# Optimization experiments

Hardware: AMD Instinct MI355X
Metric: run time of the kernel (lower is better)

Reference implementation:

```python
import jax, jax.numpy as jnp
import numpy as np

HEAD_DIM = 64
N_HEADS = 32
N_KV = 8
ROPE_BASE = 500000.0
FREQ_CONFIG = {"factor": 32.0, "low_freq_factor": 1.0, "high_freq_factor": 4.0, "original_context_length": 8192}


def _rope_tables(head_dim, theta, n_pos, fc):
    # faithful to precompute_rope_params with llama3 freq scaling
    inv_freq = 1.0 / theta ** (np.arange(0, head_dim, 2, dtype=np.float32) / head_dim)
    low_wl = fc["original_context_length"] / fc["low_freq_factor"]
    high_wl = fc["original_context_length"] / fc["high_freq_factor"]
    wavelen = 2.0 * np.pi / inv_freq
    inv_l = np.where(wavelen > low_wl, inv_freq / fc["factor"], inv_freq)
    smooth = (fc["original_context_length"] / wavelen - fc["low_freq_factor"]) / (fc["high_freq_factor"] - fc["low_freq_factor"])
    smoothed = (1.0 - smooth) * (inv_freq / fc["factor"]) + smooth * inv_freq
    med = (wavelen <= low_wl) & (wavelen >= high_wl)
    inv_freq = np.where(med, smoothed, inv_l)
    pos = np.arange(n_pos, dtype=np.float32)
    angles = pos[:, None] * inv_freq[None, :]          # [T, head_dim/2]
    angles = np.concatenate([angles, angles], axis=1)  # [T, head_dim]
    return jnp.asarray(np.cos(angles), jnp.float32), jnp.asarray(np.sin(angles), jnp.float32)


def _apply_rope(x, cos, sin):
    # x: [b, h, t, d]; cos/sin: [t, d]
    d = x.shape[-1]
    x1, x2 = x[..., : d // 2], x[..., d // 2:]
    rotated = jnp.concatenate([-x2, x1], axis=-1)
    return x * cos[None, None] + rotated * sin[None, None]


def setup_inputs() -> dict:
    key = jax.random.key(0)
    ks = jax.random.split(key, 5)
    b, t, d = 1, 2048, 2048
    s = 0.02
    return {
        "x": jax.random.normal(ks[0], (b, t, d), jnp.float32),
        "Wq": jax.random.normal(ks[1], (d, d), jnp.float32) * s,
        "Wk": jax.random.normal(ks[2], (N_KV * HEAD_DIM, d), jnp.float32) * s,
        "Wv": jax.random.normal(ks[3], (N_KV * HEAD_DIM, d), jnp.float32) * s,
        "Wo": jax.random.normal(ks[4], (d, d), jnp.float32) * s,
        "start_pos": 0,
    }


def reference(x, Wq, Wk, Wv, Wo, start_pos):
    b, t, _ = x.shape
    cos, sin = _rope_tables(HEAD_DIM, ROPE_BASE, start_pos + t, FREQ_CONFIG)
    cos, sin = cos[start_pos:start_pos + t], sin[start_pos:start_pos + t]

    q = (x @ Wq.T).reshape(b, t, N_HEADS, HEAD_DIM).transpose(0, 2, 1, 3)  # [b,H,t,d]
    k = (x @ Wk.T).reshape(b, t, N_KV, HEAD_DIM).transpose(0, 2, 1, 3)     # [b,G,t,d]
    v = (x @ Wv.T).reshape(b, t, N_KV, HEAD_DIM).transpose(0, 2, 1, 3)

    q = _apply_rope(q, cos, sin)
    k = _apply_rope(k, cos, sin)

    n_rep = N_HEADS // N_KV
    k = jnp.repeat(k, n_rep, axis=1)  # [b,H,t,d]
    v = jnp.repeat(v, n_rep, axis=1)

    scores = jnp.einsum("bhqd,bhkd->bhqk", q, k)
    causal = jnp.triu(jnp.ones((t, t), bool), k=1)
    scores = jnp.where(causal[None, None], -jnp.inf, scores) / jnp.sqrt(jnp.float32(HEAD_DIM))
    weights = jax.nn.softmax(scores, axis=-1)
    ctx = jnp.einsum("bhqk,bhkd->bhqd", weights, v)
    ctx = ctx.transpose(0, 2, 1, 3).reshape(b, t, N_HEADS * HEAD_DIM)
    return ctx @ Wo.T
```

## Files before the change

### kernel.cpp

```cpp
#include <hip/hip_runtime.h>
#include <math.h>

#define T_SEQ 2048
#define D_MODEL 2048
#define HEAD_DIM 64
#define N_HEADS 32
#define N_KV 8

using short8 = __attribute__((ext_vector_type(8))) short;
using f32x4  = __attribute__((ext_vector_type(4))) float;

#define MFMA16(a, b, c) __builtin_amdgcn_mfma_f32_16x16x32_bf16(a, b, c, 0, 0, 0)

__device__ __forceinline__ unsigned short f2bf(float f) {
    unsigned int u = __builtin_bit_cast(unsigned int, f);
    u += 0x7fff + ((u >> 16) & 1);
    return (unsigned short)(u >> 16);
}
__device__ __forceinline__ void gld_lds16(const ushort* g, ushort* l) {
    __builtin_amdgcn_global_load_lds((const __attribute__((address_space(1))) void*)g,
                                     (__attribute__((address_space(3))) void*)l, 16, 0, 0);
}

__global__ void rope_tables_kernel(float* __restrict__ cosT, float* __restrict__ sinT,
                                   const int* __restrict__ start_pos, int T) {
    int t = blockIdx.x;
    int i = threadIdx.x;
    float pos = (float)(start_pos[0] + t);
    float expo = (float)i / 32.0f;
    float inv_freq = 1.0f / powf(500000.0f, expo);
    const float two_pi = 6.283185307179586f;
    float wavelen = two_pi / inv_freq;
    const float low_wl = 8192.0f;
    const float high_wl = 2048.0f;
    float inv;
    if (wavelen > low_wl) {
        inv = inv_freq / 32.0f;
    } else if (wavelen < high_wl) {
        inv = inv_freq;
    } else {
        float smooth = (8192.0f / wavelen - 1.0f) / 3.0f;
        inv = (1.0f - smooth) * (inv_freq / 32.0f) + smooth * inv_freq;
    }
    float ang = pos * inv;
    cosT[i * T + t] = cosf(ang);
    sinT[i * T + t] = sinf(ang);
}

__global__ __launch_bounds__(256) void cast_all_kernel(
    const float* __restrict__ x, const float* __restrict__ wq,
    const float* __restrict__ wk, const float* __restrict__ wv,
    const float* __restrict__ wo,
    ushort* __restrict__ xb, ushort* __restrict__ wqb,
    ushort* __restrict__ wkb, ushort* __restrict__ wvb, ushort* __restrict__ wob) {
    int i = blockIdx.x * 256 + threadIdx.x;
    const float* src; ushort* dst; int off;
    if (i < 1048576)      { src = x;  dst = xb;  off = i; }
    else if (i < 2097152) { src = wq; dst = wqb; off = i - 1048576; }
    else if (i < 2359296) { src = wk; dst = wkb; off = i - 2097152; }
    else if (i < 2621440) { src = wv; dst = wvb; off = i - 2359296; }
    else                  { src = wo; dst = wob; off = i - 2621440; }
    float4 v = ((const float4*)src)[off];
    ushort4 o;
    o.x = f2bf(v.x); o.y = f2bf(v.y); o.z = f2bf(v.z); o.w = f2bf(v.w);
    ((ushort4*)dst)[off] = o;
}

__global__ __launch_bounds__(256) void gemm_qkv(
    const ushort* __restrict__ X, const ushort* __restrict__ Wqb,
    const ushort* __restrict__ Wkb, const ushort* __restrict__ Wvb,
    ushort* __restrict__ Qo, ushort* __restrict__ Ko, ushort* __restrict__ Vto,
    const float* __restrict__ cosT, const float* __restrict__ sinT,
    int T, int D) {
    __shared__ __align__(16) ushort As[2][2][2048];
    __shared__ __align__(16) ushort Bs[2][2][4096];
    const int tid = threadIdx.x;
    const int w = tid >> 6, l = tid & 63;
    const int m0 = blockIdx.x * 64;
    const int n0g = blockIdx.y * 128;

    const ushort* B;
    ushort* Cout;
    int n0, doRope;
    if (n0g < 2048)      { B = Wqb + (size_t)n0g * D;          Cout = Qo;  n0 = n0g;        doRope = 1; }
    else if (n0g < 2560) { B = Wkb + (size_t)(n0g - 2048) * D; Cout = Ko;  n0 = n0g - 2048; doRope = 1; }
    else                 { B = Wvb + (size_t)(n0g - 2560) * D; Cout = Vto; n0 = n0g - 2560; doRope = 0; }

    const int wm = (w >> 1) * 32, wn = (w & 1) * 64;
    const int lr = l & 15;
    const int quad = l >> 4;

    f32x4 zero = {0.f, 0.f, 0.f, 0.f};
    f32x4 acc[2][4];
#pragma unroll
    for (int i = 0; i < 2; ++i)
#pragma unroll
        for (int j = 0; j < 4; ++j) acc[i][j] = zero;

    const int srow = l >> 2;
    const int scg  = ((l & 3) ^ (srow & 3)) * 8;
    const ushort* Ag  = X + (size_t)(m0 + 16 * w + srow) * D + scg;
    const ushort* Bg0 = B + (size_t)(16 * (2 * w) + srow) * D + scg;
    const ushort* Bg1 = B + (size_t)(16 * (2 * w + 1) + srow) * D + scg;

#define GSTAGE(k0v, nb) { \
    gld_lds16(Ag  + (k0v),      &As[nb][0][w * 512]); \
    gld_lds16(Ag  + (k0v) + 32, &As[nb][1][w * 512]); \
    gld_lds16(Bg0 + (k0v),      &Bs[nb][0][(2 * w) * 512]); \
    gld_lds16(Bg0 + (k0v) + 32, &Bs[nb][1][(2 * w) * 512]); \
    gld_lds16(Bg1 + (k0v),      &Bs[nb][0][(2 * w + 1) * 512]); \
    gld_lds16(Bg1 + (k0v) + 32, &Bs[nb][1][(2 * w + 1) * 512]); }

    GSTAGE(0, 0);

    const int rsw = (quad ^ (lr & 3)) * 8;
    for (int k0 = 0; k0 < D; k0 += 64) {
        const int b = (k0 >> 6) & 1;
        __syncthreads();
        if (k0 + 64 < D) GSTAGE(k0 + 64, b ^ 1);
#pragma unroll
        for (int sub = 0; sub < 2; ++sub) {
            short8 af[2], bf[4];
#pragma unroll
            for (int i = 0; i < 2; ++i) af[i] = *(const short8*)&As[b][sub][(wm + i * 16 + lr) * 32 + rsw];
#pragma unroll
            for (int j = 0; j < 4; ++j) bf[j] = *(const short8*)&Bs[b][sub][(wn + j * 16 + lr) * 32 + rsw];
#pragma unroll
            for (int i = 0; i < 2; ++i)
#pragma unroll
                for (int j = 0; j < 4; ++j)
                    acc[i][j] = MFMA16(af[i], bf[j], acc[i][j]);
        }
    }
#undef GSTAGE

    const int mbase = m0 + wm + quad * 4;
    if (doRope) {
#pragma unroll
        for (int i = 0; i < 2; ++i) {
            int trow = mbase + i * 16;
#pragma unroll
            for (int j = 0; j < 2; ++j) {
                int i1 = lr + j * 16;
                float4 c4 = *(const float4*)&cosT[(size_t)i1 * T + trow];
                float4 s4 = *(const float4*)&sinT[(size_t)i1 * T + trow];
                int n1 = n0 + wn + lr + j * 16;
                int n2 = n1 + 32;
                size_t b1 = (size_t)(n1 >> 6) * ((size_t)T * 64) + (size_t)(n1 & 63);
                size_t b2 = (size_t)(n2 >> 6) * ((size_t)T * 64) + (size_t)(n2 & 63);
                float cs[4] = {c4.x, c4.y, c4.z, c4.w};
                float sn[4] = {s4.x, s4.y, s4.z, s4.w};
#pragma unroll
                for (int r = 0; r < 4; ++r) {
                    float x1 = acc[i][j][r], x2 = acc[i][j + 2][r];
                    Cout[b1 + (size_t)(trow + r) * 64] = f2bf(x1 * cs[r] - x2 * sn[r]);
                    Cout[b2 + (size_t)(trow + r) * 64] = f2bf(x2 * cs[r] + x1 * sn[r]);
                }
            }
        }
    } else {
#pragma unroll
        for (int i = 0; i < 2; ++i)
#pragma unroll
            for (int j = 0; j < 4; ++j) {
                int n = n0 + wn + lr + j * 16;
                int m = mbase + i * 16;
                ushort4 o;
                o.x = f2bf(acc[i][j][0]); o.y = f2bf(acc[i][j][1]);
                o.z = f2bf(acc[i][j][2]); o.w = f2bf(acc[i][j][3]);
                *(ushort4*)&Vto[(size_t)n * T + m] = o;
            }
    }
}

__global__ __launch_bounds__(256) void gemm_bt_f32(const ushort* __restrict__ A,
                                                   const ushort* __restrict__ B,
                                                   float* __restrict__ C,
                                                   int M, int N, int K) {
    __shared__ __align__(16) ushort As[2][2][2048];
    __shared__ __align__(16) ushort Bs[2][2][4096];
    const int tid = threadIdx.x;
    const int w = tid >> 6, l = tid & 63;
    const int m0 = blockIdx.x * 64, n0 = blockIdx.y * 128;
    const int wm = (w >> 1) * 32, wn = (w & 1) * 64;
    const int lr = l & 15;
    const int quad = l >> 4;

    f32x4 zero = {0.f, 0.f, 0.f, 0.f};
    f32x4 acc[2][4];
#pragma unroll
    for (int i = 0; i < 2; ++i)
#pragma unroll
        for (int j = 0; j < 4; ++j) acc[i][j] = zero;

    const int srow = l >> 2;
    const int scg  = ((l & 3) ^ (srow & 3)) * 8;
    const ushort* Ag  = A + (size_t)(m0 + 16 * w + srow) * K + scg;
    const ushort* Bg0 = B + (size_t)(n0 + 16 * (2 * w) + srow) * K + scg;
    const ushort* Bg1 = B + (size_t)(n0 + 16 * (2 * w + 1) + srow) * K + scg;

#define GSTAGE(k0v, nb) { \
    gld_lds16(Ag  + (k0v),      &As[nb][0][w * 512]); \
    gld_lds16(Ag  + (k0v) + 32, &As[nb][1][w * 512]); \
    gld_lds16(Bg0 + (k0v),      &Bs[nb][0][(2 * w) * 512]); \
    gld_lds16(Bg0 + (k0v) + 32, &Bs[nb][1][(2 * w) * 512]); \
    gld_lds16(Bg1 + (k0v),      &Bs[nb][0][(2 * w + 1) * 512]); \
    gld_lds16(Bg1 + (k0v) + 32, &Bs[nb][1][(2 * w + 1) * 512]); }

    GSTAGE(0, 0);

    const int rsw = (quad ^ (lr & 3)) * 8;
    for (int k0 = 0; k0 < K; k0 += 64) {
        const int b = (k0 >> 6) & 1;
        __syncthreads();
        if (k0 + 64 < K) GSTAGE(k0 + 64, b ^ 1);
#pragma unroll
        for (int sub = 0; sub < 2; ++sub) {
            short8 af[2], bf[4];
#pragma unroll
            for (int i = 0; i < 2; ++i) af[i] = *(const short8*)&As[b][sub][(wm + i * 16 + lr) * 32 + rsw];
#pragma unroll
            for (int j = 0; j < 4; ++j) bf[j] = *(const short8*)&Bs[b][sub][(wn + j * 16 + lr) * 32 + rsw];
#pragma unroll
            for (int i = 0; i < 2; ++i)
#pragma unroll
                for (int j = 0; j < 4; ++j)
                    acc[i][j] = MFMA16(af[i], bf[j], acc[i][j]);
        }
    }
#undef GSTAGE

    const int mbase = m0 + wm + quad * 4;
    const int nbase = n0 + wn + lr;
#pragma unroll
    for (int i = 0; i < 2; ++i)
#pragma unroll
        for (int j = 0; j < 4; ++j)
#pragma unroll
            for (int r = 0; r < 4; ++r)
                C[(size_t)(mbase + i * 16 + r) * N + (nbase + j * 16)] = acc[i][j][r];
}

__global__ __launch_bounds__(256) void attn_mfma(const ushort* __restrict__ Q,
                                                 const ushort* __restrict__ K,
                                                 const ushort* __restrict__ Vt,
                                                 ushort* __restrict__ ctx, int T) {
    __shared__ __align__(16) ushort Ks[2][4096];
    __shared__ __align__(16) ushort Vs[2][4096];
    __shared__ __align__(16) ushort Ps[4][1152];
    const int tid = threadIdx.x, w = tid >> 6, l = tid & 63;
    const int lr = l & 15, quad = l >> 4;
    const int h = blockIdx.y, hk = h >> 2;
    const ushort* Kb = K + (size_t)hk * T * 64;
    const ushort* Vb = Vt + (size_t)hk * 64 * T;

    const int srow = l >> 3;
    const int sc   = ((l & 7) ^ srow) * 8;
    const int si0 = 2 * w, si1 = 2 * w + 1;
    const int swz = lr & 7;
    f32x4 zero = {0.f, 0.f, 0.f, 0.f};

    for (int phase = 0; phase < 2; ++phase) {
        const int qt = phase == 0 ? (31 - (int)blockIdx.x) : (int)blockIdx.x;
        const int qbase = qt * 64;
        const int qrow_abs = qbase + w * 16 + lr;
        const int ntiles = qt + 1;

        short8 qf[2];
#pragma unroll
        for (int ks = 0; ks < 2; ++ks)
            qf[ks] = *(const short8*)(Q + ((size_t)h * T + qbase + w * 16 + lr) * 64 + ks * 32 + quad * 8);

        f32x4 oacc[4];
#pragma unroll
        for (int dj = 0; dj < 4; ++dj) oacc[dj] = zero;
        float lsum = 0.f;

        gld_lds16(Kb + (size_t)(8 * si0 + srow) * 64 + sc, &Ks[0][si0 * 512]);
        gld_lds16(Kb + (size_t)(8 * si1 + srow) * 64 + sc, &Ks[0][si1 * 512]);
        gld_lds16(Vb + (size_t)(8 * si0 + srow) * T + sc, &Vs[0][si0 * 512]);
        gld_lds16(Vb + (size_t)(8 * si1 + srow) * T + sc, &Vs[0][si1 * 512]);

        for (int kt = 0; kt < ntiles; ++kt) {
            const int b = kt & 1;
            __syncthreads();
            if (kt + 1 < ntiles) {
                const int k0n = (kt + 1) * 64;
                gld_lds16(Kb + (size_t)(k0n + 8 * si0 + srow) * 64 + sc, &Ks[b ^ 1][si0 * 512]);
                gld_lds16(Kb + (size_t)(k0n + 8 * si1 + srow) * 64 + sc, &Ks[b ^ 1][si1 * 512]);
                gld_lds16(Vb + (size_t)(8 * si0 + srow) * T + k0n + sc, &Vs[b ^ 1][si0 * 512]);
                gld_lds16(Vb + (size_t)(8 * si1 + srow) * T + k0n + sc, &Vs[b ^ 1][si1 * 512]);
            }
            const int k0 = kt * 64;

            f32x4 s[4];
#pragma unroll
            for (int mi = 0; mi < 4; ++mi) s[mi] = zero;
#pragma unroll
            for (int ks = 0; ks < 2; ++ks)
#pragma unroll
                for (int mi = 0; mi < 4; ++mi) {
                    short8 kf = *(const short8*)&Ks[b][(mi * 16 + lr) * 64 + ((4 * ks + quad) ^ swz) * 8];
                    s[mi] = MFMA16(kf, qf[ks], s[mi]);
                }

            const bool masked = (kt == qt);
#pragma unroll
            for (int mi = 0; mi < 4; ++mi) {
                float pv[4];
#pragma unroll
                for (int r = 0; r < 4; ++r) {
                    float p = __expf(s[mi][r] * 0.125f);
                    if (masked && (k0 + mi * 16 + quad * 4 + r > qrow_abs)) p = 0.f;
                    lsum += p;
                    pv[r] = p;
                }
                ushort4 pk;
                pk.x = f2bf(pv[0]); pk.y = f2bf(pv[1]); pk.z = f2bf(pv[2]); pk.w = f2bf(pv[3]);
                *(ushort4*)&Ps[w][lr * 72 + mi * 16 + quad * 4] = pk;
            }

#pragma unroll
            for (int ks2 = 0; ks2 < 2; ++ks2) {
                short8 pf = *(const short8*)&Ps[w][lr * 72 + ks2 * 32 + quad * 8];
#pragma unroll
                for (int dj = 0; dj < 4; ++dj) {
                    short8 vf = *(const short8*)&Vs[b][(dj * 16 + lr) * 64 + ((4 * ks2 + quad) ^ swz) * 8];
                    oacc[dj] = MFMA16(pf, vf, oacc[dj]);
                }
            }
        }

        float v = lsum;
        v += __shfl_xor(v, 16, 64);
        v += __shfl_xor(v, 32, 64);
        float invr[4];
#pragma unroll
        for (int r = 0; r < 4; ++r)
            invr[r] = 1.f / __shfl(v, quad * 4 + r, 64);

#pragma unroll
        for (int dj = 0; dj < 4; ++dj) {
            int col = h * 64 + dj * 16 + lr;
#pragma unroll
            for (int r = 0; r < 4; ++r) {
                int row = qbase + w * 16 + quad * 4 + r;
                ctx[(size_t)row * 2048 + col] = f2bf(oacc[dj][r] * invr[r]);
            }
        }
        __syncthreads();
    }
}

extern "C" void kernel_launch(void* const* d_in, const int* in_sizes, int n_in,
                              void* d_out, int out_size, void* d_ws, size_t ws_size,
                              hipStream_t stream) {
    const float* x  = (const float*)d_in[0];
    const float* Wq = (const float*)d_in[1];
    const float* Wk = (const float*)d_in[2];
    const float* Wv = (const float*)d_in[3];
    const float* Wo = (const float*)d_in[4];
    const int* start_pos = (const int*)d_in[5];
    float* out = (float*)d_out;

    const int T = T_SEQ, D = D_MODEL;
    const int KV = N_KV * HEAD_DIM;

    char* w = (char*)d_ws;
    float* cosT = (float*)w;            w += (size_t)32 * T * 4;
    float* sinT = (float*)w;            w += (size_t)32 * T * 4;
    ushort* xbf  = (ushort*)w;          w += (size_t)T * D * 2;
    ushort* wqbf = (ushort*)w;          w += (size_t)D * D * 2;
    ushort* wkbf = (ushort*)w;          w += (size_t)KV * D * 2;
    ushort* wvbf = (ushort*)w;          w += (size_t)KV * D * 2;
    ushort* wobf = (ushort*)w;          w += (size_t)D * D * 2;
    ushort* qbf  = (ushort*)w;          w += (size_t)N_HEADS * T * 64 * 2;
    ushort* kbf  = (ushort*)w;          w += (size_t)N_KV * T * 64 * 2;
    ushort* vtbf = (ushort*)w;          w += (size_t)N_KV * 64 * T * 2;
    ushort* ctxbf = xbf;

    rope_tables_kernel<<<dim3(T), dim3(32), 0, stream>>>(cosT, sinT, start_pos, T);

    cast_all_kernel<<<dim3(14336), dim3(256), 0, stream>>>(x, Wq, Wk, Wv, Wo,
                                                           xbf, wqbf, wkbf, wvbf, wobf);

    gemm_qkv<<<dim3(T / 64, (D + 2 * KV) / 128), dim3(256), 0, stream>>>(
        xbf, wqbf, wkbf, wvbf, qbf, kbf, vtbf, cosT, sinT, T, D);

    attn_mfma<<<dim3(16, N_HEADS), dim3(256), 0, stream>>>(qbf, kbf, vtbf, ctxbf, T);

    gemm_bt_f32<<<dim3(T / 64, D / 128), dim3(256), 0, stream>>>(ctxbf, wobf, out, T, D, D);
}
```

Baseline: 213.8 us.

## Rewrite attention with 32x32 MFMA, register-resident P, and folded softmax scale

Moves the attention kernel from 16x16x32 to 32x32x16 bf16 MFMA with 2 waves per block, each owning 32 query rows. P stays in registers: it is packed with v_cvt_pk_bf16_f32 and rearranged with permlane32_swap, removing the LDS round-trip for probabilities. The 1/sqrt(d)*log2(e) factor is folded into Q in the QKV GEMM epilogue so the softmax can use exp2 directly. The grid changes from phased two-tile blocks to one q-tile per block, with head-dependent ordering for load balance. The rope-table kernel is also relaunched with 256-thread blocks.

```diff
diff --git a/kernel.cpp b/kernel.cpp
--- a/kernel.cpp
+++ b/kernel.cpp
@@ -9,8 +9,11 @@
 
 using short8 = __attribute__((ext_vector_type(8))) short;
 using f32x4  = __attribute__((ext_vector_type(4))) float;
+using f32x16 = __attribute__((ext_vector_type(16))) float;
+using u32x4  = __attribute__((ext_vector_type(4))) unsigned int;
 
 #define MFMA16(a, b, c) __builtin_amdgcn_mfma_f32_16x16x32_bf16(a, b, c, 0, 0, 0)
+#define MFMA32(a, b, c) __builtin_amdgcn_mfma_f32_32x32x16_bf16(a, b, c, 0, 0, 0)
 
 __device__ __forceinline__ unsigned short f2bf(float f) {
     unsigned int u = __builtin_bit_cast(unsigned int, f);
@@ -21,11 +24,22 @@
     __builtin_amdgcn_global_load_lds((const __attribute__((address_space(1))) void*)g,
                                      (__attribute__((address_space(3))) void*)l, 16, 0, 0);
 }
-
-__global__ void rope_tables_kernel(float* __restrict__ cosT, float* __restrict__ sinT,
-                                   const int* __restrict__ start_pos, int T) {
-    int t = blockIdx.x;
-    int i = threadIdx.x;
+__device__ __forceinline__ unsigned int cvtpk(float lo, float hi) {
+    unsigned int r;
+    asm("v_cvt_pk_bf16_f32 %0, %1, %2" : "=v"(r) : "v"(lo), "v"(hi));
+    return r;
+}
+__device__ __forceinline__ void plswap(unsigned int& a, unsigned int& b) {
+    auto r = __builtin_amdgcn_permlane32_swap(a, b, false, false);
+    a = r[0];
+    b = r[1];
+}
+
+__global__ __launch_bounds__(256) void rope_tables_kernel(float* __restrict__ cosT, float* __restrict__ sinT,
+                                                          const int* __restrict__ start_pos, int T) {
+    int idx = blockIdx.x * 256 + threadIdx.x;
+    int t = idx >> 5;
+    int i = idx & 31;
     float pos = (float)(start_pos[0] + t);
     float expo = (float)i / 32.0f;
     float inv_freq = 1.0f / powf(500000.0f, expo);
@@ -136,6 +150,7 @@
 
     const int mbase = m0 + wm + quad * 4;
     if (doRope) {
+        const float qsc = (n0g < 2048) ? 0.18033688011112042f : 1.0f;
 #pragma unroll
         for (int i = 0; i < 2; ++i) {
             int trow = mbase + i * 16;
@@ -153,8 +168,8 @@
 #pragma unroll
                 for (int r = 0; r < 4; ++r) {
                     float x1 = acc[i][j][r], x2 = acc[i][j + 2][r];
-                    Cout[b1 + (size_t)(trow + r) * 64] = f2bf(x1 * cs[r] - x2 * sn[r]);
-                    Cout[b2 + (size_t)(trow + r) * 64] = f2bf(x2 * cs[r] + x1 * sn[r]);
+                    Cout[b1 + (size_t)(trow + r) * 64] = f2bf((x1 * cs[r] - x2 * sn[r]) * qsc);
+                    Cout[b2 + (size_t)(trow + r) * 64] = f2bf((x2 * cs[r] + x1 * sn[r]) * qsc);
                 }
             }
         }
@@ -241,114 +256,120 @@
                 C[(size_t)(mbase + i * 16 + r) * N + (nbase + j * 16)] = acc[i][j][r];
 }
 
-__global__ __launch_bounds__(256) void attn_mfma(const ushort* __restrict__ Q,
-                                                 const ushort* __restrict__ K,
-                                                 const ushort* __restrict__ Vt,
-                                                 ushort* __restrict__ ctx, int T) {
+__global__ __launch_bounds__(128, 2) void attn_mfma(const ushort* __restrict__ Q,
+                                                    const ushort* __restrict__ K,
+                                                    const ushort* __restrict__ Vt,
+                                                    ushort* __restrict__ ctx, int T) {
     __shared__ __align__(16) ushort Ks[2][4096];
     __shared__ __align__(16) ushort Vs[2][4096];
-    __shared__ __align__(16) ushort Ps[4][1152];
     const int tid = threadIdx.x, w = tid >> 6, l = tid & 63;
-    const int lr = l & 15, quad = l >> 4;
+    const int lq = l & 31, hi = l >> 5;
     const int h = blockIdx.y, hk = h >> 2;
+    const int qb = ((h >> 3) & 1) ? (31 - (int)blockIdx.x) : (int)blockIdx.x;
+    const int ntiles = qb + 1;
     const ushort* Kb = K + (size_t)hk * T * 64;
     const ushort* Vb = Vt + (size_t)hk * 64 * T;
 
     const int srow = l >> 3;
     const int sc   = ((l & 7) ^ srow) * 8;
-    const int si0 = 2 * w, si1 = 2 * w + 1;
-    const int swz = lr & 7;
-    f32x4 zero = {0.f, 0.f, 0.f, 0.f};
-
-    for (int phase = 0; phase < 2; ++phase) {
-        const int qt = phase == 0 ? (31 - (int)blockIdx.x) : (int)blockIdx.x;
-        const int qbase = qt * 64;
-        const int qrow_abs = qbase + w * 16 + lr;
-        const int ntiles = qt + 1;
-
-        short8 qf[2];
-#pragma unroll
-        for (int ks = 0; ks < 2; ++ks)
-            qf[ks] = *(const short8*)(Q + ((size_t)h * T + qbase + w * 16 + lr) * 64 + ks * 32 + quad * 8);
-
-        f32x4 oacc[4];
-#pragma unroll
-        for (int dj = 0; dj < 4; ++dj) oacc[dj] = zero;
-        float lsum = 0.f;
-
-        gld_lds16(Kb + (size_t)(8 * si0 + srow) * 64 + sc, &Ks[0][si0 * 512]);
-        gld_lds16(Kb + (size_t)(8 * si1 + srow) * 64 + sc, &Ks[0][si1 * 512]);
-        gld_lds16(Vb + (size_t)(8 * si0 + srow) * T + sc, &Vs[0][si0 * 512]);
-        gld_lds16(Vb + (size_t)(8 * si1 + srow) * T + sc, &Vs[0][si1 * 512]);
-
-        for (int kt = 0; kt < ntiles; ++kt) {
-            const int b = kt & 1;
-            __syncthreads();
-            if (kt + 1 < ntiles) {
-                const int k0n = (kt + 1) * 64;
-                gld_lds16(Kb + (size_t)(k0n + 8 * si0 + srow) * 64 + sc, &Ks[b ^ 1][si0 * 512]);
-                gld_lds16(Kb + (size_t)(k0n + 8 * si1 + srow) * 64 + sc, &Ks[b ^ 1][si1 * 512]);
-                gld_lds16(Vb + (size_t)(8 * si0 + srow) * T + k0n + sc, &Vs[b ^ 1][si0 * 512]);
-                gld_lds16(Vb + (size_t)(8 * si1 + srow) * T + k0n + sc, &Vs[b ^ 1][si1 * 512]);
+
+    const ushort* Qrow = Q + ((size_t)h * T + qb * 64 + w * 32 + lq) * 64;
+    short8 qf[4];
+#pragma unroll
+    for (int ks = 0; ks < 4; ++ks)
+        qf[ks] = *(const short8*)(Qrow + ks * 16 + hi * 8);
+
+    f32x16 oacc0, oacc1;
+#pragma unroll
+    for (int r = 0; r < 16; ++r) { oacc0[r] = 0.f; oacc1[r] = 0.f; }
+    float ls[4] = {0.f, 0.f, 0.f, 0.f};
+    const int limit = w * 32 + lq;
+
+#define ASTAGE(kt, buf) do { \
+    size_t _k0 = (size_t)(kt) * 64; \
+    const int _s0 = w * 4; \
+    gld_lds16(Kb + (_k0 + _s0 * 8      + srow) * 64 + sc, &Ks[buf][(_s0    ) * 512]); \
+    gld_lds16(Kb + (_k0 + _s0 * 8 + 8  + srow) * 64 + sc, &Ks[buf][(_s0 + 1) * 512]); \
+    gld_lds16(Kb + (_k0 + _s0 * 8 + 16 + srow) * 64 + sc, &Ks[buf][(_s0 + 2) * 512]); \
+    gld_lds16(Kb + (_k0 + _s0 * 8 + 24 + srow) * 64 + sc, &Ks[buf][(_s0 + 3) * 512]); \
+    gld_lds16(Vb + (size_t)(_s0 * 8      + srow) * T + _k0 + sc, &Vs[buf][(_s0    ) * 512]); \
+    gld_lds16(Vb + (size_t)(_s0 * 8 + 8  + srow) * T + _k0 + sc, &Vs[buf][(_s0 + 1) * 512]); \
+    gld_lds16(Vb + (size_t)(_s0 * 8 + 16 + srow) * T + _k0 + sc, &Vs[buf][(_s0 + 2) * 512]); \
+    gld_lds16(Vb + (size_t)(_s0 * 8 + 24 + srow) * T + _k0 + sc, &Vs[buf][(_s0 + 3) * 512]); \
+} while (0)
+
+    ASTAGE(0, 0);
+
+    for (int kt = 0; kt < ntiles; ++kt) {
+        const int b = kt & 1;
+        __syncthreads();
+        if (kt + 1 < ntiles) ASTAGE(kt + 1, b ^ 1);
+
+        f32x16 s0, s1;
+#pragma unroll
+        for (int r = 0; r < 16; ++r) { s0[r] = 0.f; s1[r] = 0.f; }
+#pragma unroll
+        for (int ks = 0; ks < 4; ++ks) {
+            const int c = ((ks * 2 + hi) ^ (lq & 7)) * 8;
+            short8 kf0 = *(const short8*)&Ks[b][lq * 64 + c];
+            short8 kf1 = *(const short8*)&Ks[b][(lq + 32) * 64 + c];
+            s0 = MFMA32(kf0, qf[ks], s0);
+            s1 = MFMA32(kf1, qf[ks], s1);
+        }
+
+        f32x16 p0, p1;
+        if (kt == ntiles - 1) {
+#pragma unroll
+            for (int r = 0; r < 16; ++r) {
+                const int kk = (r & 3) + 8 * (r >> 2) + 4 * hi;
+                p0[r] = (kk <= limit)      ? __builtin_amdgcn_exp2f(s0[r]) : 0.f;
+                p1[r] = (kk + 32 <= limit) ? __builtin_amdgcn_exp2f(s1[r]) : 0.f;
             }
-            const int k0 = kt * 64;
-
-            f32x4 s[4];
-#pragma unroll
-            for (int mi = 0; mi < 4; ++mi) s[mi] = zero;
-#pragma unroll
-            for (int ks = 0; ks < 2; ++ks)
-#pragma unroll
-                for (int mi = 0; mi < 4; ++mi) {
-                    short8 kf = *(const short8*)&Ks[b][(mi * 16 + lr) * 64 + ((4 * ks + quad) ^ swz) * 8];
-                    s[mi] = MFMA16(kf, qf[ks], s[mi]);
-                }
-
-            const bool masked = (kt == qt);
-#pragma unroll
-            for (int mi = 0; mi < 4; ++mi) {
-                float pv[4];
-#pragma unroll
-                for (int r = 0; r < 4; ++r) {
-                    float p = __expf(s[mi][r] * 0.125f);
-                    if (masked && (k0 + mi * 16 + quad * 4 + r > qrow_abs)) p = 0.f;
-                    lsum += p;
-                    pv[r] = p;
-                }
-                ushort4 pk;
-                pk.x = f2bf(pv[0]); pk.y = f2bf(pv[1]); pk.z = f2bf(pv[2]); pk.w = f2bf(pv[3]);
-                *(ushort4*)&Ps[w][lr * 72 + mi * 16 + quad * 4] = pk;
+        } else {
+#pragma unroll
+            for (int r = 0; r < 16; ++r) {
+                p0[r] = __builtin_amdgcn_exp2f(s0[r]);
+                p1[r] = __builtin_amdgcn_exp2f(s1[r]);
             }
-
-#pragma unroll
-            for (int ks2 = 0; ks2 < 2; ++ks2) {
-                short8 pf = *(const short8*)&Ps[w][lr * 72 + ks2 * 32 + quad * 8];
-#pragma unroll
-                for (int dj = 0; dj < 4; ++dj) {
-                    short8 vf = *(const short8*)&Vs[b][(dj * 16 + lr) * 64 + ((4 * ks2 + quad) ^ swz) * 8];
-                    oacc[dj] = MFMA16(pf, vf, oacc[dj]);
-                }
-            }
-        }
-
-        float v = lsum;
-        v += __shfl_xor(v, 16, 64);
-        v += __shfl_xor(v, 32, 64);
-        float invr[4];
-#pragma unroll
-        for (int r = 0; r < 4; ++r)
-            invr[r] = 1.f / __shfl(v, quad * 4 + r, 64);
-
-#pragma unroll
-        for (int dj = 0; dj < 4; ++dj) {
-            int col = h * 64 + dj * 16 + lr;
-#pragma unroll
-            for (int r = 0; r < 4; ++r) {
-                int row = qbase + w * 16 + quad * 4 + r;
-                ctx[(size_t)row * 2048 + col] = f2bf(oacc[dj][r] * invr[r]);
-            }
-        }
-        __syncthreads();
+        }
+#pragma unroll
+        for (int r = 0; r < 16; ++r) ls[r & 3] += p0[r] + p1[r];
+
+#pragma unroll
+        for (int ks2 = 0; ks2 < 4; ++ks2) {
+            const f32x16& pp = (ks2 < 2) ? p0 : p1;
+            const int bse = (ks2 & 1) * 8;
+            unsigned int a0 = cvtpk(pp[bse + 0], pp[bse + 1]);
+            unsigned int a1 = cvtpk(pp[bse + 2], pp[bse + 3]);
+            unsigned int b0 = cvtpk(pp[bse + 4], pp[bse + 5]);
+            unsigned int b1 = cvtpk(pp[bse + 6], pp[bse + 7]);
+            plswap(a0, b0);
+            plswap(a1, b1);
+            u32x4 tw = {a0, a1, b0, b1};
+            short8 pf = __builtin_bit_cast(short8, tw);
+            const int c = ((ks2 * 2 + hi) ^ (lq & 7)) * 8;
+            short8 vf0 = *(const short8*)&Vs[b][lq * 64 + c];
+            short8 vf1 = *(const short8*)&Vs[b][(lq + 32) * 64 + c];
+            oacc0 = MFMA32(vf0, pf, oacc0);
+            oacc1 = MFMA32(vf1, pf, oacc1);
+        }
+    }
+#undef ASTAGE
+
+    float vsum = (ls[0] + ls[1]) + (ls[2] + ls[3]);
+    vsum += __shfl_xor(vsum, 32, 64);
+    const float inv = 1.f / vsum;
+
+    ushort* cp = ctx + (size_t)(qb * 64 + w * 32 + lq) * 2048 + h * 64;
+#pragma unroll
+    for (int g = 0; g < 4; ++g) {
+        ushort4 o0, o1;
+        o0.x = f2bf(oacc0[4 * g + 0] * inv); o0.y = f2bf(oacc0[4 * g + 1] * inv);
+        o0.z = f2bf(oacc0[4 * g + 2] * inv); o0.w = f2bf(oacc0[4 * g + 3] * inv);
+        *(ushort4*)&cp[g * 8 + hi * 4] = o0;
+        o1.x = f2bf(oacc1[4 * g + 0] * inv); o1.y = f2bf(oacc1[4 * g + 1] * inv);
+        o1.z = f2bf(oacc1[4 * g + 2] * inv); o1.w = f2bf(oacc1[4 * g + 3] * inv);
+        *(ushort4*)&cp[32 + g * 8 + hi * 4] = o1;
     }
 }
 
@@ -379,7 +400,7 @@
     ushort* vtbf = (ushort*)w;          w += (size_t)N_KV * 64 * T * 2;
     ushort* ctxbf = xbf;
 
-    rope_tables_kernel<<<dim3(T), dim3(32), 0, stream>>>(cosT, sinT, start_pos, T);
+    rope_tables_kernel<<<dim3((T * 32) / 256), dim3(256), 0, stream>>>(cosT, sinT, start_pos, T);
 
     cast_all_kernel<<<dim3(14336), dim3(256), 0, stream>>>(x, Wq, Wk, Wv, Wo,
                                                            xbf, wqbf, wkbf, wvbf, wobf);
@@ -387,7 +408,7 @@
     gemm_qkv<<<dim3(T / 64, (D + 2 * KV) / 128), dim3(256), 0, stream>>>(
         xbf, wqbf, wkbf, wvbf, qbf, kbf, vtbf, cosT, sinT, T, D);
 
-    attn_mfma<<<dim3(16, N_HEADS), dim3(256), 0, stream>>>(qbf, kbf, vtbf, ctxbf, T);
+    attn_mfma<<<dim3(32, N_HEADS), dim3(128), 0, stream>>>(qbf, kbf, vtbf, ctxbf, T);
 
     gemm_bt_f32<<<dim3(T / 64, D / 128), dim3(256), 0, stream>>>(ctxbf, wobf, out, T, D, D);
 }
```

New measurement: 205.4 us. 1.04x faster.
